# Kernel tuning notes

Hardware: AMD Instinct MI355X
Metric: run time of the kernel (lower is better)

Reference implementation:

```python
import jax, jax.numpy as jnp
import numpy as np

B, T, F = 16, 1024, 512       # batch, time, input_dim
G, V, D = 2, 320, 128         # num_groups, num_vars, var_dim (quantized_dim // G)
TAU = 2.0                     # max_temp * decay**0 at num_updates=0
EPS = 1e-7


def setup_inputs() -> dict:
    key = jax.random.key(0)
    kx, kw, kc, kg = jax.random.split(key, 4)
    x = jax.random.normal(kx, (B, T, F), dtype=jnp.float32)
    w_proj = jax.random.normal(kw, (G * V, F), dtype=jnp.float32)  # NormalLinear: std=1
    b_proj = jnp.zeros((G * V,), dtype=jnp.float32)
    codebook = jax.random.uniform(kc, (1, G * V, D), dtype=jnp.float32)  # uniform init
    u = jax.random.uniform(kg, (B * T, G, V), dtype=jnp.float32, minval=1e-10, maxval=1.0)
    gumbel = -jnp.log(-jnp.log(u))
    return {"x": x, "w_proj": w_proj, "b_proj": b_proj, "codebook": codebook, "gumbel": gumbel}


def reference(x, w_proj, b_proj, codebook, gumbel):
    bsz, tsz, _ = x.shape
    # projection -> (B, T, G, V)
    logits = (jnp.einsum("btf,nf->btn", x, w_proj) + b_proj).reshape(bsz, tsz, G, V)

    # hard one-hot of argmax (float32), like scatter_
    k = jnp.argmax(logits, axis=-1)
    hard_x = jax.nn.one_hot(k, V, dtype=jnp.float32)  # (B, T, G, V)

    # code perplexity: mean over batch dim only, sum over (T, G)
    hard_probs = hard_x.mean(axis=0)  # (T, G, V)
    code_perplexity = jnp.exp(-jnp.sum(hard_probs * jnp.log(hard_probs + EPS), axis=-1)).sum()

    # prob perplexity: softmax over codes, mean over all tokens, sum over groups
    flat_logits = logits.reshape(bsz * tsz, G, V)
    avg_probs = jax.nn.softmax(flat_logits, axis=-1).mean(axis=0)  # (G, V)
    prob_perplexity = jnp.exp(-jnp.sum(avg_probs * jnp.log(avg_probs + EPS), axis=-1)).sum()

    # gumbel-softmax, hard=True with straight-through estimator (training path)
    y_soft = jax.nn.softmax((flat_logits + gumbel) / TAU, axis=-1)  # (N, G, V)
    idx = jnp.argmax(y_soft, axis=-1)
    y_hard = jax.nn.one_hot(idx, V, dtype=y_soft.dtype)
    y = y_hard + y_soft - jax.lax.stop_gradient(y_soft)  # (N, G, V)

    # broadcast-multiply + sum over codes == grouped gather/matmul against codebook
    cb_gvd = codebook.reshape(G, V, D)
    quantized = jnp.einsum("ngv,gvd->ngd", y, cb_gvd).reshape(bsz, tsz, G * D)
    return quantized, code_perplexity, prob_perplexity
```

## Files before the change

### kernel.cpp

```cpp
#include <hip/hip_runtime.h>
#include <math.h>

#define B_   16
#define T_   1024
#define F_   512
#define G_   2
#define V_   320
#define D_   128
#define N_   (B_ * T_)
#define GV   (G_ * V_)
#define EPS_ 1e-7f

#define ROWS    64
#define THREADS 512
#define NBLK    (N_ / ROWS)
#define NC      32

#define BOFF  0
#define AOFF  40960
#define BUFSZ 45056
#define LDSZ  (3 * BUFSZ)

typedef _Float16 half8 __attribute__((ext_vector_type(8)));
typedef _Float16 half2_t __attribute__((ext_vector_type(2)));
typedef float f32x16 __attribute__((ext_vector_type(16)));

#define GLDS16(g, l)                                                           \
  __builtin_amdgcn_global_load_lds(                                            \
      (const __attribute__((address_space(1))) unsigned int*)(g),              \
      (__attribute__((address_space(3))) unsigned int*)(l), 16, 0, 0)

#define CNTW      (T_ * G_ * (V_ / 2))
#define WS_COUNTS 0
#define WS_AVG    CNTW
#define WS_ENT    (WS_AVG + NBLK * GV)
#define WS_WPK    (WS_ENT + T_ * G_)
#define WS_AVGRED (WS_WPK + (GV * F_ * 2 / 2))

__global__ __launch_bounds__(640) void k_conv_w(
    const float* __restrict__ w, _Float16* __restrict__ wpk,
    unsigned* __restrict__ counts)
{
  const int cl = blockIdx.x;
  const int c = cl >> 1, limb = cl & 1;
#pragma unroll
  for (int z = 0; z < 8; ++z)
    counts[(size_t)z * 40960 + blockIdx.x * 640 + threadIdx.x] = 0u;
#pragma unroll
  for (int it = 0; it < 2; ++it) {
    const int t2 = threadIdx.x + it * 640;
    const int m = t2 >> 6, ln = t2 & 63;
    const int row = m * 32 + (ln & 31);
    const int k0 = c * 16 + (ln >> 5) * 8;
    const float4 v0 = *(const float4*)(w + (size_t)row * F_ + k0);
    const float4 v1 = *(const float4*)(w + (size_t)row * F_ + k0 + 4);
    half8 h;
#pragma unroll
    for (int k = 0; k < 8; ++k) {
      const float vk = (k < 4) ? ((const float*)&v0)[k] : ((const float*)&v1)[k - 4];
      const _Float16 hk = (_Float16)vk;
      h[k] = limb ? (_Float16)((vk - (float)hk) * 2048.0f) : hk;
    }
    ((half8*)wpk)[((size_t)cl * 20 + m) * 64 + ln] = h;
  }
}

__global__ __launch_bounds__(THREADS, 1) void k_fused(
    const float* __restrict__ x, const _Float16* __restrict__ wpk,
    const float* __restrict__ bias, const float* __restrict__ cb,
    const float* __restrict__ gum, float* __restrict__ out,
    unsigned* __restrict__ counts, float* __restrict__ avg_part)
{
  __shared__ __align__(16) unsigned char SB[LDSZ];
  const int tid = threadIdx.x;
  const int wv  = tid >> 6;
  const int ln  = tid & 63;
  const int lo  = ln & 31, hi = ln >> 5;
  const int wvm = wv >> 2, wvn = wv & 3;
  const int blk = blockIdx.x;
  const int n0  = blk * ROWS;

  f32x16 ah_acc[5], al_acc[5];
#pragma unroll
  for (int t = 0; t < 5; ++t)
#pragma unroll
    for (int i = 0; i < 16; ++i) { ah_acc[t][i] = 0.0f; al_acc[t][i] = 0.0f; }

  const int arow = tid >> 3;
  const int akp  = tid & 7;
  const int awoff = (arow >> 5) * 1024 + (((akp >> 2) << 5) + (arow & 31)) * 16
                  + (akp & 3) * 4;
  const float2* x2 = (const float2*)x;
  const size_t xrowbase = (size_t)(n0 + arow) * (F_ / 2) + akp;

  const int aro_h = AOFF + 0 * 2048 + wvm * 1024 + ln * 16;
  const int aro_l = AOFF + 1 * 2048 + wvm * 1024 + ln * 16;
  int bro_h[5], bro_l[5];
#pragma unroll
  for (int t = 0; t < 5; ++t) {
    bro_h[t] = BOFF + (0 * 20 + wvn * 5 + t) * 1024 + ln * 16;
    bro_l[t] = BOFF + (1 * 20 + wvn * 5 + t) * 1024 + ln * 16;
  }

  auto STAGE_B = [&](int c, unsigned char* buf) {
#pragma unroll
    for (int i = 0; i < 5; ++i) {
      const int seg = wv * 5 + i;
      GLDS16(wpk + ((size_t)(c * 40 + seg) * 64 + ln) * 8, buf + BOFF + seg * 1024);
    }
  };
  auto STAGE_A = [&](float2 xv, unsigned char* buf) {
    half2_t hh, hl;
#pragma unroll
    for (int k = 0; k < 2; ++k) {
      const float f = k ? xv.y : xv.x;
      const _Float16 h = (_Float16)f;
      hh[k] = h; hl[k] = (_Float16)((f - (float)h) * 2048.0f);
    }
    *(half2_t*)(buf + AOFF + awoff) = hh;
    *(half2_t*)(buf + AOFF + 2048 + awoff) = hl;
  };

  unsigned char* b0 = SB;
  unsigned char* b1 = SB + BUFSZ;
  unsigned char* b2 = SB + 2 * BUFSZ;

  STAGE_B(0, b0);
  const float2 xv0 = x2[xrowbase + 0 * 8];
  STAGE_B(1, b1);
  float2 xcur = x2[xrowbase + 1 * 8];
  STAGE_A(xv0, b0);
  __builtin_amdgcn_sched_barrier(0);
  asm volatile("s_waitcnt vmcnt(6) lgkmcnt(0)" ::: "memory");
  __builtin_amdgcn_s_barrier();
  __builtin_amdgcn_sched_barrier(0);

  for (int cc = 0; cc < NC; ++cc) {
    float2 xnew = xcur;
    if (cc + 2 < NC) {
      STAGE_B(cc + 2, b2);
      xnew = x2[xrowbase + (cc + 2) * 8];
    }
    if (cc + 1 < NC) STAGE_A(xcur, b1);
    {
      const half8 ahf = *(const half8*)(b0 + aro_h);
      const half8 alf = *(const half8*)(b0 + aro_l);
#pragma unroll
      for (int t = 0; t < 5; ++t) {
        const half8 bh = *(const half8*)(b0 + bro_h[t]);
        const half8 bl = *(const half8*)(b0 + bro_l[t]);
        ah_acc[t] = __builtin_amdgcn_mfma_f32_32x32x16_f16(ahf, bh, ah_acc[t], 0, 0, 0);
        al_acc[t] = __builtin_amdgcn_mfma_f32_32x32x16_f16(alf, bh, al_acc[t], 0, 0, 0);
        al_acc[t] = __builtin_amdgcn_mfma_f32_32x32x16_f16(ahf, bl, al_acc[t], 0, 0, 0);
      }
    }
    unsigned char* tmp = b0; b0 = b1; b1 = b2; b2 = tmp;
    xcur = xnew;
    __builtin_amdgcn_sched_barrier(0);
    if (cc + 2 < NC)
      asm volatile("s_waitcnt vmcnt(6) lgkmcnt(0)" ::: "memory");
    else
      asm volatile("s_waitcnt vmcnt(0) lgkmcnt(0)" ::: "memory");
    __builtin_amdgcn_s_barrier();
    __builtin_amdgcn_sched_barrier(0);
  }

  float bfrag[5];
#pragma unroll
  for (int t = 0; t < 5; ++t) bfrag[t] = bias[wvn * 160 + t * 32 + lo];

  float racc[G_][5];
#pragma unroll
  for (int g = 0; g < G_; ++g)
#pragma unroll
    for (int j = 0; j < 5; ++j) racc[g][j] = 0.f;

  float* LBUF = (float*)SB;

#pragma unroll
  for (int R = 0; R < 4; ++R) {
    if (wvm == (R >> 1)) {
#pragma unroll
      for (int t = 0; t < 5; ++t) {
        const int col = wvn * 160 + t * 32 + lo;
#pragma unroll
        for (int rr = 0; rr < 8; ++rr) {
          const int reg  = ((R & 1) << 3) + rr;
          const int lrow = (rr & 3) + ((rr >> 2) << 3) + (hi << 2);
          LBUF[lrow * GV + col] =
              ah_acc[t][reg] + al_acc[t][reg] * (1.0f / 2048.0f) + bfrag[t];
        }
      }
    }
    __syncthreads();
#pragma unroll
    for (int rr2 = 0; rr2 < 2; ++rr2) {
      const int lrow = wv * 2 + rr2;
      const int n = n0 + R * 16 + lrow;
#pragma unroll
      for (int g = 0; g < G_; ++g) {
        float L[5], GU[5];
#pragma unroll
        for (int j = 0; j < 5; ++j) {
          L[j]  = LBUF[lrow * GV + g * V_ + 64 * j + ln];
          GU[j] = gum[(size_t)n * GV + g * V_ + 64 * j + ln];
        }
        float m1 = L[0];         int a1 = ln;
        float m2 = L[0] + GU[0]; int a2 = ln;
#pragma unroll
        for (int j = 1; j < 5; ++j) {
          const int cix = 64 * j + ln;
          if (L[j] > m1) { m1 = L[j]; a1 = cix; }
          const float t2 = L[j] + GU[j];
          if (t2 > m2) { m2 = t2; a2 = cix; }
        }
        for (int off = 32; off; off >>= 1) {
          float om = __shfl_down(m1, off); int oa = __shfl_down(a1, off);
          if (om > m1 || (om == m1 && oa < a1)) { m1 = om; a1 = oa; }
          float om2 = __shfl_down(m2, off); int oa2 = __shfl_down(a2, off);
          if (om2 > m2 || (om2 == m2 && oa2 < a2)) { m2 = om2; a2 = oa2; }
        }
        m1 = __shfl(m1, 0); a1 = __shfl(a1, 0); a2 = __shfl(a2, 0);

        float e[5], s = 0.f;
#pragma unroll
        for (int j = 0; j < 5; ++j) { e[j] = expf(L[j] - m1); s += e[j]; }
        for (int off = 32; off; off >>= 1) s += __shfl_down(s, off);
        s = __shfl(s, 0);
        const float inv = 1.0f / s;
#pragma unroll
        for (int j = 0; j < 5; ++j) racc[g][j] += e[j] * inv;

        if (ln == 0) {
          const int t = n & (T_ - 1);
          atomicAdd(&counts[(t * G_ + g) * (V_ / 2) + (a1 >> 1)],
                    1u << ((a1 & 1) * 16));
        }
        const float2* cbr = (const float2*)(cb + (size_t)(g * V_ + a2) * D_);
        float2* op = (float2*)(out + (size_t)n * (G_ * D_) + g * D_);
        op[ln] = cbr[ln];
      }
    }
    __syncthreads();
  }

  float* la = (float*)SB;
#pragma unroll
  for (int g = 0; g < G_; ++g)
#pragma unroll
    for (int j = 0; j < 5; ++j)
      la[wv * GV + g * V_ + 64 * j + ln] = racc[g][j];
  __syncthreads();
  for (int cix = tid; cix < GV; cix += THREADS) {
    float s = 0.f;
#pragma unroll
    for (int v = 0; v < 8; ++v) s += la[v * GV + cix];
    avg_part[(size_t)blk * GV + cix] = s;
  }
}

__global__ __launch_bounds__(256) void k_post(
    const unsigned* __restrict__ counts, float* __restrict__ ent,
    const float* __restrict__ avg_part, float* __restrict__ avgred)
{
  const int b = blockIdx.x;
  const int lane = threadIdx.x & 63;
  if (b < (T_ * G_) / 4) {
    const int item = b * 4 + (threadIdx.x >> 6);
    const unsigned* c = counts + (size_t)item * (V_ / 2);
    float s = 0.f;
#pragma unroll
    for (int j = 0; j < 3; ++j) {
      const int wi = lane + 64 * j;
      if (wi < V_ / 2) {
        const unsigned wd = c[wi];
        const float h0 = (float)(wd & 0xffffu) * (1.0f / B_);
        const float h1 = (float)(wd >> 16) * (1.0f / B_);
        s += h0 * logf(h0 + EPS_) + h1 * logf(h1 + EPS_);
      }
    }
    for (int off = 32; off; off >>= 1) s += __shfl_down(s, off);
    if (lane == 0) ent[item] = expf(-s);
  } else {
    const int cix = (b - (T_ * G_) / 4) * 4 + (threadIdx.x >> 6);
    float s = 0.f;
    for (int bb = lane; bb < NBLK; bb += 64) s += avg_part[(size_t)bb * GV + cix];
    for (int off = 32; off; off >>= 1) s += __shfl_down(s, off);
    if (lane == 0) avgred[cix] = s;
  }
}

__global__ __launch_bounds__(GV) void k_final(
    const float* __restrict__ avgred, const float* __restrict__ ent,
    float* __restrict__ out2)
{
  __shared__ float sh[GV];
  __shared__ float shc[GV];
  const int tid = threadIdx.x;

  const float p = avgred[tid] * (1.0f / N_);
  sh[tid] = p * logf(p + EPS_);

  float cs = 0.f;
  for (int i = tid; i < T_ * G_; i += GV) cs += ent[i];
  shc[tid] = cs;
  __syncthreads();

  if (tid < 64) {
    float s0 = 0.f, s1 = 0.f, sc = 0.f;
    for (int j = tid; j < V_; j += 64) { s0 += sh[j]; s1 += sh[V_ + j]; }
    for (int j = tid; j < GV; j += 64) sc += shc[j];
    for (int off = 32; off; off >>= 1) {
      s0 += __shfl_down(s0, off);
      s1 += __shfl_down(s1, off);
      sc += __shfl_down(sc, off);
    }
    if (tid == 0) {
      out2[0] = sc;
      out2[1] = expf(-s0) + expf(-s1);
    }
  }
}

extern "C" void kernel_launch(void* const* d_in, const int* in_sizes, int n_in,
                              void* d_out, int out_size, void* d_ws, size_t ws_size,
                              hipStream_t stream) {
  const float* x   = (const float*)d_in[0];
  const float* w   = (const float*)d_in[1];
  const float* b   = (const float*)d_in[2];
  const float* cb  = (const float*)d_in[3];
  const float* gum = (const float*)d_in[4];
  float* out = (float*)d_out;
  float* ws  = (float*)d_ws;

  unsigned* counts = (unsigned*)(ws + WS_COUNTS);
  float* avgp   = ws + WS_AVG;
  float* ent    = ws + WS_ENT;
  _Float16* wpk = (_Float16*)(ws + WS_WPK);
  float* avgred = ws + WS_AVGRED;

  k_conv_w<<<64, 640, 0, stream>>>(w, wpk, counts);
  k_fused<<<NBLK, THREADS, 0, stream>>>(x, wpk, b, cb, gum, out, counts, avgp);
  k_post<<<(T_ * G_) / 4 + GV / 4, 256, 0, stream>>>(counts, ent, avgp, avgred);
  k_final<<<1, GV, 0, stream>>>(avgred, ent, out + (size_t)N_ * G_ * D_);
}
```

Measured before the change: 181.1 us.

## Load GEMM operands directly from global into registers, dropping LDS staging

```diff
diff --git a/kernel.cpp b/kernel.cpp
--- a/kernel.cpp
+++ b/kernel.cpp
@@ -16,19 +16,8 @@
 #define NBLK    (N_ / ROWS)
 #define NC      32
 
-#define BOFF  0
-#define AOFF  40960
-#define BUFSZ 45056
-#define LDSZ  (3 * BUFSZ)
-
 typedef _Float16 half8 __attribute__((ext_vector_type(8)));
-typedef _Float16 half2_t __attribute__((ext_vector_type(2)));
 typedef float f32x16 __attribute__((ext_vector_type(16)));
-
-#define GLDS16(g, l)                                                           \
-  __builtin_amdgcn_global_load_lds(                                            \
-      (const __attribute__((address_space(1))) unsigned int*)(g),              \
-      (__attribute__((address_space(3))) unsigned int*)(l), 16, 0, 0)
 
 #define CNTW      (T_ * G_ * (V_ / 2))
 #define WS_COUNTS 0
@@ -71,7 +60,7 @@
     const float* __restrict__ gum, float* __restrict__ out,
     unsigned* __restrict__ counts, float* __restrict__ avg_part)
 {
-  __shared__ __align__(16) unsigned char SB[LDSZ];
+  __shared__ float SB2[16 * GV];
   const int tid = threadIdx.x;
   const int wv  = tid >> 6;
   const int ln  = tid & 63;
@@ -86,83 +75,46 @@
 #pragma unroll
     for (int i = 0; i < 16; ++i) { ah_acc[t][i] = 0.0f; al_acc[t][i] = 0.0f; }
 
-  const int arow = tid >> 3;
-  const int akp  = tid & 7;
-  const int awoff = (arow >> 5) * 1024 + (((akp >> 2) << 5) + (arow & 31)) * 16
-                  + (akp & 3) * 4;
-  const float2* x2 = (const float2*)x;
-  const size_t xrowbase = (size_t)(n0 + arow) * (F_ / 2) + akp;
-
-  const int aro_h = AOFF + 0 * 2048 + wvm * 1024 + ln * 16;
-  const int aro_l = AOFF + 1 * 2048 + wvm * 1024 + ln * 16;
-  int bro_h[5], bro_l[5];
+  const half8* wbase = (const half8*)wpk + (size_t)(wvn * 5) * 64 + ln;
+  const float* xrow  = x + (size_t)(n0 + wvm * 32 + lo) * F_ + hi * 8;
+
+  half8 wch[5], wcl[5];
 #pragma unroll
   for (int t = 0; t < 5; ++t) {
-    bro_h[t] = BOFF + (0 * 20 + wvn * 5 + t) * 1024 + ln * 16;
-    bro_l[t] = BOFF + (1 * 20 + wvn * 5 + t) * 1024 + ln * 16;
-  }
-
-  auto STAGE_B = [&](int c, unsigned char* buf) {
-#pragma unroll
-    for (int i = 0; i < 5; ++i) {
-      const int seg = wv * 5 + i;
-      GLDS16(wpk + ((size_t)(c * 40 + seg) * 64 + ln) * 8, buf + BOFF + seg * 1024);
-    }
-  };
-  auto STAGE_A = [&](float2 xv, unsigned char* buf) {
-    half2_t hh, hl;
-#pragma unroll
-    for (int k = 0; k < 2; ++k) {
-      const float f = k ? xv.y : xv.x;
+    wch[t] = wbase[(size_t)(0 * 20 + t) * 64];
+    wcl[t] = wbase[(size_t)(1 * 20 + t) * 64];
+  }
+  float4 xc0 = *(const float4*)(xrow + 0);
+  float4 xc1 = *(const float4*)(xrow + 4);
+
+  for (int cc = 0; cc < NC; ++cc) {
+    const int c1 = (cc + 1 < NC) ? cc + 1 : cc;
+    half8 wnh[5], wnl[5];
+#pragma unroll
+    for (int t = 0; t < 5; ++t) {
+      wnh[t] = wbase[((size_t)(c1 * 2 + 0) * 20 + t) * 64];
+      wnl[t] = wbase[((size_t)(c1 * 2 + 1) * 20 + t) * 64];
+    }
+    const float4 xn0 = *(const float4*)(xrow + c1 * 16);
+    const float4 xn1 = *(const float4*)(xrow + c1 * 16 + 4);
+
+    half8 xh8, xl8;
+#pragma unroll
+    for (int k = 0; k < 8; ++k) {
+      const float f = (k < 4) ? ((const float*)&xc0)[k] : ((const float*)&xc1)[k - 4];
       const _Float16 h = (_Float16)f;
-      hh[k] = h; hl[k] = (_Float16)((f - (float)h) * 2048.0f);
-    }
-    *(half2_t*)(buf + AOFF + awoff) = hh;
-    *(half2_t*)(buf + AOFF + 2048 + awoff) = hl;
-  };
-
-  unsigned char* b0 = SB;
-  unsigned char* b1 = SB + BUFSZ;
-  unsigned char* b2 = SB + 2 * BUFSZ;
-
-  STAGE_B(0, b0);
-  const float2 xv0 = x2[xrowbase + 0 * 8];
-  STAGE_B(1, b1);
-  float2 xcur = x2[xrowbase + 1 * 8];
-  STAGE_A(xv0, b0);
-  __builtin_amdgcn_sched_barrier(0);
-  asm volatile("s_waitcnt vmcnt(6) lgkmcnt(0)" ::: "memory");
-  __builtin_amdgcn_s_barrier();
-  __builtin_amdgcn_sched_barrier(0);
-
-  for (int cc = 0; cc < NC; ++cc) {
-    float2 xnew = xcur;
-    if (cc + 2 < NC) {
-      STAGE_B(cc + 2, b2);
-      xnew = x2[xrowbase + (cc + 2) * 8];
-    }
-    if (cc + 1 < NC) STAGE_A(xcur, b1);
-    {
-      const half8 ahf = *(const half8*)(b0 + aro_h);
-      const half8 alf = *(const half8*)(b0 + aro_l);
-#pragma unroll
-      for (int t = 0; t < 5; ++t) {
-        const half8 bh = *(const half8*)(b0 + bro_h[t]);
-        const half8 bl = *(const half8*)(b0 + bro_l[t]);
-        ah_acc[t] = __builtin_amdgcn_mfma_f32_32x32x16_f16(ahf, bh, ah_acc[t], 0, 0, 0);
-        al_acc[t] = __builtin_amdgcn_mfma_f32_32x32x16_f16(alf, bh, al_acc[t], 0, 0, 0);
-        al_acc[t] = __builtin_amdgcn_mfma_f32_32x32x16_f16(ahf, bl, al_acc[t], 0, 0, 0);
-      }
-    }
-    unsigned char* tmp = b0; b0 = b1; b1 = b2; b2 = tmp;
-    xcur = xnew;
-    __builtin_amdgcn_sched_barrier(0);
-    if (cc + 2 < NC)
-      asm volatile("s_waitcnt vmcnt(6) lgkmcnt(0)" ::: "memory");
-    else
-      asm volatile("s_waitcnt vmcnt(0) lgkmcnt(0)" ::: "memory");
-    __builtin_amdgcn_s_barrier();
-    __builtin_amdgcn_sched_barrier(0);
+      xh8[k] = h;
+      xl8[k] = (_Float16)((f - (float)h) * 2048.0f);
+    }
+#pragma unroll
+    for (int t = 0; t < 5; ++t) {
+      ah_acc[t] = __builtin_amdgcn_mfma_f32_32x32x16_f16(xh8, wch[t], ah_acc[t], 0, 0, 0);
+      al_acc[t] = __builtin_amdgcn_mfma_f32_32x32x16_f16(xl8, wch[t], al_acc[t], 0, 0, 0);
+      al_acc[t] = __builtin_amdgcn_mfma_f32_32x32x16_f16(xh8, wcl[t], al_acc[t], 0, 0, 0);
+    }
+#pragma unroll
+    for (int t = 0; t < 5; ++t) { wch[t] = wnh[t]; wcl[t] = wnl[t]; }
+    xc0 = xn0; xc1 = xn1;
   }
 
   float bfrag[5];
@@ -175,7 +127,7 @@
 #pragma unroll
     for (int j = 0; j < 5; ++j) racc[g][j] = 0.f;
 
-  float* LBUF = (float*)SB;
+  float* LBUF = SB2;
 
 #pragma unroll
   for (int R = 0; R < 4; ++R) {
@@ -244,7 +196,7 @@
     __syncthreads();
   }
 
-  float* la = (float*)SB;
+  float* la = SB2;
 #pragma unroll
   for (int g = 0; g < G_; ++g)
 #pragma unroll
```

After: 185.8 us. +2.6%, slower.
